# Kernel optimization log

Hardware: AMD Instinct MI355X
Metric: run time of the kernel (lower is better)

The kernel has to match this reference:

```python
import jax, jax.numpy as jnp
import numpy as np

N_EMBED = 768
NUM_HEADS = 12
HEAD_DIM = N_EMBED // NUM_HEADS
B, L = 4, 2048


def setup_inputs() -> dict:
    key = jax.random.key(0)
    ks = jax.random.split(key, 11)
    s = 0.02
    return {
        "key": jax.random.normal(ks[0], (B, L, N_EMBED), jnp.float32),
        "query": jax.random.normal(ks[1], (B, L, N_EMBED), jnp.float32),
        "value": jax.random.normal(ks[2], (B, L, N_EMBED), jnp.float32),
        "Wk": jax.random.normal(ks[3], (N_EMBED, N_EMBED), jnp.float32) * s,
        "bk": jnp.zeros((N_EMBED,), jnp.float32),
        "Wq": jax.random.normal(ks[4], (N_EMBED, N_EMBED), jnp.float32) * s,
        "bq": jnp.zeros((N_EMBED,), jnp.float32),
        "Wv": jax.random.normal(ks[5], (N_EMBED, N_EMBED), jnp.float32) * s,
        "bv": jnp.zeros((N_EMBED,), jnp.float32),
        "Wfc": jax.random.normal(ks[6], (N_EMBED, N_EMBED), jnp.float32) * s,
        "bfc": jnp.zeros((N_EMBED,), jnp.float32),
    }


def reference(key, query, value, Wk, bk, Wq, bq, Wv, bv, Wfc, bfc):
    # Linear projections (torch Linear: x @ W.T + b)
    k = key @ Wk.T + bk      # [B, Lk, D]
    q = query @ Wq.T + bq    # [B, Lq, D]
    v = value @ Wv.T + bv    # [B, Lv, D]
    Bsz, Lq = q.shape[0], q.shape[1]
    k = k.reshape(Bsz, -1, NUM_HEADS, HEAD_DIM)
    q = q.reshape(Bsz, Lq, NUM_HEADS, HEAD_DIM)
    v = v.reshape(Bsz, -1, NUM_HEADS, HEAD_DIM)
    # Full [B, H, Lq, Lk] score tensor, scaled by sqrt(n_embed) (faithful to source)
    energies = jnp.einsum("nqhd,nkhd->nhqk", q, k)
    attn = jax.nn.softmax(energies / jnp.sqrt(jnp.float32(N_EMBED)), axis=3)
    out = jnp.einsum("nhql,nlhd->nqhd", attn, v).reshape(Bsz, Lq, N_EMBED)
    return out @ Wfc.T + bfc
```

## Files before the change

### kernel.cpp

```cpp
#include <hip/hip_runtime.h>
#include <hip/hip_bf16.h>

#define NEMB 768
#define NH   12
#define HD   64
#define BSZ  4
#define SEQ  2048
#define MTOT (BSZ * SEQ)

typedef short bf16x8 __attribute__((ext_vector_type(8)));
typedef short short4v __attribute__((ext_vector_type(4)));
typedef float f32x4 __attribute__((ext_vector_type(4)));

__device__ __forceinline__ short f2bf(float f) {
  unsigned u = __builtin_bit_cast(unsigned, f);
  u += 0x7FFFu + ((u >> 16) & 1u);
  return (short)(u >> 16);
}

__device__ __forceinline__ void g2l16(const short* g, short* l) {
  __builtin_amdgcn_global_load_lds((const __attribute__((address_space(1))) unsigned*)g,
                                   (__attribute__((address_space(3))) unsigned*)l, 16, 0, 0);
}

__device__ __forceinline__ int swz(int x) { return (x ^ (x >> 3)) & 7; }

__global__ __launch_bounds__(256) void cvt3(const float* __restrict__ a0, const float* __restrict__ a1,
                                            const float* __restrict__ a2, short* __restrict__ o0,
                                            short* __restrict__ o1, short* __restrict__ o2) {
  const float* in; short* out;
  switch (blockIdx.y) { case 0: in = a0; out = o0; break;
                        case 1: in = a1; out = o1; break;
                        default: in = a2; out = o2; }
  int i = blockIdx.x * 256 + threadIdx.x;
  float4 f = reinterpret_cast<const float4*>(in)[i];
  short4v s; s[0] = f2bf(f.x); s[1] = f2bf(f.y); s[2] = f2bf(f.z); s[3] = f2bf(f.w);
  reinterpret_cast<short4v*>(out)[i] = s;
}

__global__ __launch_bounds__(256) void cvt4(const float* __restrict__ a0, const float* __restrict__ a1,
                                            const float* __restrict__ a2, const float* __restrict__ a3,
                                            short* __restrict__ o0, short* __restrict__ o1,
                                            short* __restrict__ o2, short* __restrict__ o3) {
  const float* in; short* out;
  switch (blockIdx.y) { case 0: in = a0; out = o0; break;
                        case 1: in = a1; out = o1; break;
                        case 2: in = a2; out = o2; break;
                        default: in = a3; out = o3; }
  int i = blockIdx.x * 256 + threadIdx.x;
  float4 f = reinterpret_cast<const float4*>(in)[i];
  short4v s; s[0] = f2bf(f.x); s[1] = f2bf(f.y); s[2] = f2bf(f.z); s[3] = f2bf(f.w);
  reinterpret_cast<short4v*>(out)[i] = s;
}

template <int OUTBF>
__global__ __launch_bounds__(256) void gemm_nt(const short* __restrict__ A, const short* __restrict__ W,
                                               const float* __restrict__ bias, void* __restrict__ Cout) {
  __shared__ __align__(16) short As[128 * 32];
  __shared__ __align__(16) short Bs[128 * 32];
  const int tid = threadIdx.x;
  const int lane = tid & 63, w = tid >> 6;
  const int wr = w >> 1, wc = w & 1;
  const int l15 = lane & 15, l4 = lane >> 4;
  const int m0 = blockIdx.x * 128, n0 = blockIdx.y * 128;

  f32x4 acc[4][4] = {};

  for (int k0 = 0; k0 < NEMB; k0 += 32) {
    __syncthreads();
#pragma unroll
    for (int i = 0; i < 2; ++i) {
      const int idx = tid + i * 256;
      const int row = idx >> 2, u = idx & 3;
      g2l16(A + (size_t)(m0 + row) * NEMB + k0 + u * 8, &As[idx * 8]);
      g2l16(W + (size_t)(n0 + row) * NEMB + k0 + u * 8, &Bs[idx * 8]);
    }
    __syncthreads();

    bf16x8 af[4], bfr[4];
#pragma unroll
    for (int m = 0; m < 4; ++m)
      af[m] = *reinterpret_cast<const bf16x8*>(&As[(wr * 64 + m * 16 + l15) * 32 + l4 * 8]);
#pragma unroll
    for (int n = 0; n < 4; ++n)
      bfr[n] = *reinterpret_cast<const bf16x8*>(&Bs[(wc * 64 + n * 16 + l15) * 32 + l4 * 8]);
#pragma unroll
    for (int m = 0; m < 4; ++m)
#pragma unroll
      for (int n = 0; n < 4; ++n)
        acc[m][n] = __builtin_amdgcn_mfma_f32_16x16x32_bf16(af[m], bfr[n], acc[m][n], 0, 0, 0);
  }

  float bj[4];
#pragma unroll
  for (int n = 0; n < 4; ++n) bj[n] = bias[n0 + wc * 64 + n * 16 + l15];
#pragma unroll
  for (int m = 0; m < 4; ++m)
#pragma unroll
    for (int n = 0; n < 4; ++n) {
      const int col = n0 + wc * 64 + n * 16 + l15;
#pragma unroll
      for (int r = 0; r < 4; ++r) {
        const int row = m0 + wr * 64 + m * 16 + l4 * 4 + r;
        const float v = acc[m][n][r] + bj[n];
        if (OUTBF) reinterpret_cast<short*>(Cout)[(size_t)row * NEMB + col] = f2bf(v);
        else       reinterpret_cast<float*>(Cout)[(size_t)row * NEMB + col] = v;
      }
    }
}

__global__ __launch_bounds__(256) void attn_mfma(const short* __restrict__ qp, const short* __restrict__ kp,
                                                 const short* __restrict__ vp, short* __restrict__ ao) {
  __shared__ __align__(16) short Ks[64 * 64];
  __shared__ __align__(16) short Vt[64 * 64];
  __shared__ __align__(16) short Ps[4][16 * 72];
  const int tid = threadIdx.x, lane = tid & 63, w = tid >> 6;
  const int l15 = lane & 15, l4 = lane >> 4;
  const int q0 = blockIdx.x * 64;
  const int bh = blockIdx.y, b = bh / NH, h = bh % NH;
  const size_t abase = (size_t)b * SEQ * NEMB + h * HD;

  bf16x8 qf[2];
#pragma unroll
  for (int kb = 0; kb < 2; ++kb)
    qf[kb] = *reinterpret_cast<const bf16x8*>(
        &qp[abase + (size_t)(q0 + w * 16 + l15) * NEMB + kb * 32 + l4 * 8]);

  f32x4 o[4] = {};
  float lacc[4] = {0.f, 0.f, 0.f, 0.f};
  const float scale = 0.036084391824351615f;
  const int vd8 = tid & 7, vkv2 = tid >> 3;

  for (int kt = 0; kt < SEQ / 64; ++kt) {
    __syncthreads();
#pragma unroll
    for (int i = 0; i < 2; ++i) {
      const int idx = tid + i * 256;
      const int row = idx >> 3, u = idx & 7;
      g2l16(kp + abase + (size_t)(kt * 64 + row) * NEMB + (u ^ swz(row)) * 8, &Ks[idx * 8]);
    }
    {
      const short* vr = vp + abase + (size_t)(kt * 64 + vkv2 * 2) * NEMB + vd8 * 8;
      bf16x8 v0 = *reinterpret_cast<const bf16x8*>(vr);
      bf16x8 v1 = *reinterpret_cast<const bf16x8*>(vr + NEMB);
      const int u = vkv2 >> 2, sub = vkv2 & 3;
#pragma unroll
      for (int j = 0; j < 8; ++j) {
        const int d = vd8 * 8 + j;
        unsigned pack = (unsigned)(unsigned short)v0[j] | ((unsigned)(unsigned short)v1[j] << 16);
        *reinterpret_cast<unsigned*>(reinterpret_cast<char*>(Vt) + d * 128 + (u ^ swz(d)) * 16 + sub * 4) = pack;
      }
    }
    __syncthreads();

    f32x4 sf[4];
#pragma unroll
    for (int nf = 0; nf < 4; ++nf) {
      f32x4 a = {0.f, 0.f, 0.f, 0.f};
#pragma unroll
      for (int kb = 0; kb < 2; ++kb) {
        const int row = nf * 16 + l15;
        const int u = kb * 4 + l4;
        bf16x8 kf = *reinterpret_cast<const bf16x8*>(
            reinterpret_cast<char*>(Ks) + row * 128 + (u ^ swz(row)) * 16);
        a = __builtin_amdgcn_mfma_f32_16x16x32_bf16(qf[kb], kf, a, 0, 0, 0);
      }
      sf[nf] = a;
    }

#pragma unroll
    for (int nf = 0; nf < 4; ++nf)
#pragma unroll
      for (int r = 0; r < 4; ++r) {
        const float p = __expf(sf[nf][r] * scale);
        lacc[r] += p;
        Ps[w][(l4 * 4 + r) * 72 + nf * 16 + l15] = f2bf(p);
      }

#pragma unroll
    for (int kb = 0; kb < 2; ++kb) {
      bf16x8 pf = *reinterpret_cast<const bf16x8*>(&Ps[w][l15 * 72 + kb * 32 + l4 * 8]);
#pragma unroll
      for (int df = 0; df < 4; ++df) {
        const int d = df * 16 + l15;
        const int u = kb * 4 + l4;
        bf16x8 vf = *reinterpret_cast<const bf16x8*>(
            reinterpret_cast<char*>(Vt) + d * 128 + (u ^ swz(d)) * 16);
        o[df] = __builtin_amdgcn_mfma_f32_16x16x32_bf16(pf, vf, o[df], 0, 0, 0);
      }
    }
  }

#pragma unroll
  for (int r = 0; r < 4; ++r)
#pragma unroll
    for (int off = 1; off < 16; off <<= 1)
      lacc[r] += __shfl_xor(lacc[r], off, 64);

#pragma unroll
  for (int df = 0; df < 4; ++df)
#pragma unroll
    for (int r = 0; r < 4; ++r) {
      const int row = q0 + w * 16 + l4 * 4 + r;
      ao[abase + (size_t)row * NEMB + df * 16 + l15] = f2bf(o[df][r] / lacc[r]);
    }
}

extern "C" void kernel_launch(void* const* d_in, const int* in_sizes, int n_in,
                              void* d_out, int out_size, void* d_ws, size_t ws_size,
                              hipStream_t stream) {
  const float* key   = (const float*)d_in[0];
  const float* query = (const float*)d_in[1];
  const float* value = (const float*)d_in[2];
  const float* Wk    = (const float*)d_in[3];
  const float* bk    = (const float*)d_in[4];
  const float* Wq    = (const float*)d_in[5];
  const float* bq    = (const float*)d_in[6];
  const float* Wv    = (const float*)d_in[7];
  const float* bv    = (const float*)d_in[8];
  const float* Wfc   = (const float*)d_in[9];
  const float* bfc   = (const float*)d_in[10];

  const size_t P = (size_t)MTOT * NEMB;
  const size_t WSZ = (size_t)NEMB * NEMB;
  short* ws  = (short*)d_ws;
  short* qb  = ws;
  short* kb2 = qb + P;
  short* vb2 = kb2 + P;
  short* wq  = vb2 + P;
  short* wk  = wq + WSZ;
  short* wv  = wk + WSZ;
  short* wf  = wv + WSZ;
  short* qpp = wf + WSZ;
  short* kpp = qpp + P;
  short* vpp = kpp + P;
  short* aop = vpp + P;

  cvt3<<<dim3(P / 4 / 256, 3), 256, 0, stream>>>(query, key, value, qb, kb2, vb2);
  cvt4<<<dim3(WSZ / 4 / 256, 4), 256, 0, stream>>>(Wq, Wk, Wv, Wfc, wq, wk, wv, wf);

  dim3 gg(MTOT / 128, NEMB / 128);
  gemm_nt<1><<<gg, 256, 0, stream>>>(qb,  wq, bq, qpp);
  gemm_nt<1><<<gg, 256, 0, stream>>>(kb2, wk, bk, kpp);
  gemm_nt<1><<<gg, 256, 0, stream>>>(vb2, wv, bv, vpp);
  attn_mfma<<<dim3(SEQ / 64, BSZ * NH), 256, 0, stream>>>(qpp, kpp, vpp, aop);
  gemm_nt<0><<<gg, 256, 0, stream>>>(aop, wf, bfc, d_out);
}
```

Baseline: 322.4 us.

## Merge launches, fold softmax scale into Q projection, and swizzle attention LDS

Collapses the two conversion kernels into one launch and the three QKV projection GEMMs into a single z-indexed launch. The softmax scale times log2(e) is folded into the Q projection epilogue so attention can use exp2f directly. Attention also gets an XCD-aware block remap, V loads issued before the barrier, perm-based V transpose packing, an XOR-swizzled P buffer to cut LDS bank conflicts, and a reciprocal instead of a per-element divide. Rounding Q after scaling slightly changes numerics, and the merged conversion grid launches many idle blocks for the weight matrices.

```diff
diff --git a/kernel.cpp b/kernel.cpp
--- a/kernel.cpp
+++ b/kernel.cpp
@@ -1,5 +1,6 @@
 #include <hip/hip_runtime.h>
 #include <hip/hip_bf16.h>
+#include <math.h>
 
 #define NEMB 768
 #define NH   12
@@ -8,14 +9,16 @@
 #define SEQ  2048
 #define MTOT (BSZ * SEQ)
 
+#define SCALE_LOG2E 0.0520587833f
+
 typedef short bf16x8 __attribute__((ext_vector_type(8)));
 typedef short short4v __attribute__((ext_vector_type(4)));
 typedef float f32x4 __attribute__((ext_vector_type(4)));
+typedef unsigned u32x4 __attribute__((ext_vector_type(4)));
 
 __device__ __forceinline__ short f2bf(float f) {
-  unsigned u = __builtin_bit_cast(unsigned, f);
-  u += 0x7FFFu + ((u >> 16) & 1u);
-  return (short)(u >> 16);
+  __bf16 h = (__bf16)f;
+  return __builtin_bit_cast(short, h);
 }
 
 __device__ __forceinline__ void g2l16(const short* g, short* l) {
@@ -25,37 +28,97 @@
 
 __device__ __forceinline__ int swz(int x) { return (x ^ (x >> 3)) & 7; }
 
-__global__ __launch_bounds__(256) void cvt3(const float* __restrict__ a0, const float* __restrict__ a1,
-                                            const float* __restrict__ a2, short* __restrict__ o0,
-                                            short* __restrict__ o1, short* __restrict__ o2) {
-  const float* in; short* out;
-  switch (blockIdx.y) { case 0: in = a0; out = o0; break;
-                        case 1: in = a1; out = o1; break;
-                        default: in = a2; out = o2; }
+__global__ __launch_bounds__(256) void cvt_all(
+    const float* __restrict__ i0, const float* __restrict__ i1, const float* __restrict__ i2,
+    const float* __restrict__ i3, const float* __restrict__ i4, const float* __restrict__ i5,
+    const float* __restrict__ i6,
+    short* __restrict__ o0, short* __restrict__ o1, short* __restrict__ o2,
+    short* __restrict__ o3, short* __restrict__ o4, short* __restrict__ o5,
+    short* __restrict__ o6) {
+  const int ACT4 = (MTOT * NEMB) / 4;
+  const int WGT4 = (NEMB * NEMB) / 4;
+  const float* in; short* out; int n4;
+  switch (blockIdx.y) {
+    case 0: in = i0; out = o0; n4 = ACT4; break;
+    case 1: in = i1; out = o1; n4 = ACT4; break;
+    case 2: in = i2; out = o2; n4 = ACT4; break;
+    case 3: in = i3; out = o3; n4 = WGT4; break;
+    case 4: in = i4; out = o4; n4 = WGT4; break;
+    case 5: in = i5; out = o5; n4 = WGT4; break;
+    default: in = i6; out = o6; n4 = WGT4; break;
+  }
   int i = blockIdx.x * 256 + threadIdx.x;
+  if (i >= n4) return;
   float4 f = reinterpret_cast<const float4*>(in)[i];
   short4v s; s[0] = f2bf(f.x); s[1] = f2bf(f.y); s[2] = f2bf(f.z); s[3] = f2bf(f.w);
   reinterpret_cast<short4v*>(out)[i] = s;
 }
 
-__global__ __launch_bounds__(256) void cvt4(const float* __restrict__ a0, const float* __restrict__ a1,
-                                            const float* __restrict__ a2, const float* __restrict__ a3,
-                                            short* __restrict__ o0, short* __restrict__ o1,
-                                            short* __restrict__ o2, short* __restrict__ o3) {
-  const float* in; short* out;
-  switch (blockIdx.y) { case 0: in = a0; out = o0; break;
-                        case 1: in = a1; out = o1; break;
-                        case 2: in = a2; out = o2; break;
-                        default: in = a3; out = o3; }
-  int i = blockIdx.x * 256 + threadIdx.x;
-  float4 f = reinterpret_cast<const float4*>(in)[i];
-  short4v s; s[0] = f2bf(f.x); s[1] = f2bf(f.y); s[2] = f2bf(f.z); s[3] = f2bf(f.w);
-  reinterpret_cast<short4v*>(out)[i] = s;
-}
-
-template <int OUTBF>
-__global__ __launch_bounds__(256) void gemm_nt(const short* __restrict__ A, const short* __restrict__ W,
-                                               const float* __restrict__ bias, void* __restrict__ Cout) {
+__global__ __launch_bounds__(256) void gemm_qkv(
+    const short* __restrict__ A0, const short* __restrict__ A1, const short* __restrict__ A2,
+    const short* __restrict__ W0, const short* __restrict__ W1, const short* __restrict__ W2,
+    const float* __restrict__ b0, const float* __restrict__ b1, const float* __restrict__ b2,
+    short* __restrict__ O0, short* __restrict__ O1, short* __restrict__ O2) {
+  __shared__ __align__(16) short As[128 * 32];
+  __shared__ __align__(16) short Bs[128 * 32];
+  const short* A; const short* W; const float* bias; short* O; float scl;
+  switch (blockIdx.z) {
+    case 0:  A = A0; W = W0; bias = b0; O = O0; scl = SCALE_LOG2E; break;
+    case 1:  A = A1; W = W1; bias = b1; O = O1; scl = 1.f; break;
+    default: A = A2; W = W2; bias = b2; O = O2; scl = 1.f; break;
+  }
+  const int tid = threadIdx.x;
+  const int lane = tid & 63, w = tid >> 6;
+  const int wr = w >> 1, wc = w & 1;
+  const int l15 = lane & 15, l4 = lane >> 4;
+  const int m0 = blockIdx.x * 128, n0 = blockIdx.y * 128;
+
+  f32x4 acc[4][4] = {};
+
+  for (int k0 = 0; k0 < NEMB; k0 += 32) {
+    __syncthreads();
+#pragma unroll
+    for (int i = 0; i < 2; ++i) {
+      const int idx = tid + i * 256;
+      const int row = idx >> 2, u = idx & 3;
+      g2l16(A + (size_t)(m0 + row) * NEMB + k0 + u * 8, &As[idx * 8]);
+      g2l16(W + (size_t)(n0 + row) * NEMB + k0 + u * 8, &Bs[idx * 8]);
+    }
+    __syncthreads();
+
+    bf16x8 af[4], bfr[4];
+#pragma unroll
+    for (int m = 0; m < 4; ++m)
+      af[m] = *reinterpret_cast<const bf16x8*>(&As[(wr * 64 + m * 16 + l15) * 32 + l4 * 8]);
+#pragma unroll
+    for (int n = 0; n < 4; ++n)
+      bfr[n] = *reinterpret_cast<const bf16x8*>(&Bs[(wc * 64 + n * 16 + l15) * 32 + l4 * 8]);
+#pragma unroll
+    for (int m = 0; m < 4; ++m)
+#pragma unroll
+      for (int n = 0; n < 4; ++n)
+        acc[m][n] = __builtin_amdgcn_mfma_f32_16x16x32_bf16(af[m], bfr[n], acc[m][n], 0, 0, 0);
+  }
+
+  float bj[4];
+#pragma unroll
+  for (int n = 0; n < 4; ++n) bj[n] = bias[n0 + wc * 64 + n * 16 + l15];
+#pragma unroll
+  for (int m = 0; m < 4; ++m)
+#pragma unroll
+    for (int n = 0; n < 4; ++n) {
+      const int col = n0 + wc * 64 + n * 16 + l15;
+#pragma unroll
+      for (int r = 0; r < 4; ++r) {
+        const int row = m0 + wr * 64 + m * 16 + l4 * 4 + r;
+        O[(size_t)row * NEMB + col] = f2bf((acc[m][n][r] + bj[n]) * scl);
+      }
+    }
+}
+
+__global__ __launch_bounds__(256) void gemm_fc(
+    const short* __restrict__ A, const short* __restrict__ W,
+    const float* __restrict__ bias, float* __restrict__ C) {
   __shared__ __align__(16) short As[128 * 32];
   __shared__ __align__(16) short Bs[128 * 32];
   const int tid = threadIdx.x;
@@ -102,9 +165,7 @@
 #pragma unroll
       for (int r = 0; r < 4; ++r) {
         const int row = m0 + wr * 64 + m * 16 + l4 * 4 + r;
-        const float v = acc[m][n][r] + bj[n];
-        if (OUTBF) reinterpret_cast<short*>(Cout)[(size_t)row * NEMB + col] = f2bf(v);
-        else       reinterpret_cast<float*>(Cout)[(size_t)row * NEMB + col] = v;
+        C[(size_t)row * NEMB + col] = acc[m][n][r] + bj[n];
       }
     }
 }
@@ -116,8 +177,11 @@
   __shared__ __align__(16) short Ps[4][16 * 72];
   const int tid = threadIdx.x, lane = tid & 63, w = tid >> 6;
   const int l15 = lane & 15, l4 = lane >> 4;
-  const int q0 = blockIdx.x * 64;
-  const int bh = blockIdx.y, b = bh / NH, h = bh % NH;
+  const int wg = blockIdx.x;
+  const int nid = (wg & 7) * 192 + (wg >> 3);
+  const int q0 = (nid & 31) * 64;
+  const int bh = nid >> 5;
+  const int b = bh / NH, h = bh - b * NH;
   const size_t abase = (size_t)b * SEQ * NEMB + h * HD;
 
   bf16x8 qf[2];
@@ -128,11 +192,16 @@
 
   f32x4 o[4] = {};
   float lacc[4] = {0.f, 0.f, 0.f, 0.f};
-  const float scale = 0.036084391824351615f;
   const int vd8 = tid & 7, vkv2 = tid >> 3;
+  const int vu = vkv2 >> 2, vsub = vkv2 & 3;
+  const int pch = l15 >> 3, pcl = l15 & 7;
 
   for (int kt = 0; kt < SEQ / 64; ++kt) {
-    __syncthreads();
+    const short* vr = vp + abase + (size_t)(kt * 64 + vkv2 * 2) * NEMB + vd8 * 8;
+    bf16x8 v0 = *reinterpret_cast<const bf16x8*>(vr);
+    bf16x8 v1 = *reinterpret_cast<const bf16x8*>(vr + NEMB);
+    __syncthreads();
+
 #pragma unroll
     for (int i = 0; i < 2; ++i) {
       const int idx = tid + i * 256;
@@ -140,15 +209,15 @@
       g2l16(kp + abase + (size_t)(kt * 64 + row) * NEMB + (u ^ swz(row)) * 8, &Ks[idx * 8]);
     }
     {
-      const short* vr = vp + abase + (size_t)(kt * 64 + vkv2 * 2) * NEMB + vd8 * 8;
-      bf16x8 v0 = *reinterpret_cast<const bf16x8*>(vr);
-      bf16x8 v1 = *reinterpret_cast<const bf16x8*>(vr + NEMB);
-      const int u = vkv2 >> 2, sub = vkv2 & 3;
-#pragma unroll
-      for (int j = 0; j < 8; ++j) {
-        const int d = vd8 * 8 + j;
-        unsigned pack = (unsigned)(unsigned short)v0[j] | ((unsigned)(unsigned short)v1[j] << 16);
-        *reinterpret_cast<unsigned*>(reinterpret_cast<char*>(Vt) + d * 128 + (u ^ swz(d)) * 16 + sub * 4) = pack;
+      u32x4 a0 = __builtin_bit_cast(u32x4, v0);
+      u32x4 a1 = __builtin_bit_cast(u32x4, v1);
+#pragma unroll
+      for (int jj = 0; jj < 4; ++jj) {
+        unsigned lo = __builtin_amdgcn_perm(a1[jj], a0[jj], 0x05040100u);
+        unsigned hi = __builtin_amdgcn_perm(a1[jj], a0[jj], 0x07060302u);
+        const int d0 = vd8 * 8 + jj * 2;
+        *reinterpret_cast<unsigned*>(reinterpret_cast<char*>(Vt) + d0 * 128 + (vu ^ swz(d0)) * 16 + vsub * 4) = lo;
+        *reinterpret_cast<unsigned*>(reinterpret_cast<char*>(Vt) + (d0 + 1) * 128 + (vu ^ swz(d0 + 1)) * 16 + vsub * 4) = hi;
       }
     }
     __syncthreads();
@@ -172,14 +241,15 @@
     for (int nf = 0; nf < 4; ++nf)
 #pragma unroll
       for (int r = 0; r < 4; ++r) {
-        const float p = __expf(sf[nf][r] * scale);
+        const float p = exp2f(sf[nf][r]);
         lacc[r] += p;
-        Ps[w][(l4 * 4 + r) * 72 + nf * 16 + l15] = f2bf(p);
+        Ps[w][(l4 * 4 + r) * 72 + (((nf * 2 + pch) ^ l4) << 3) + pcl] = f2bf(p);
       }
 
 #pragma unroll
     for (int kb = 0; kb < 2; ++kb) {
-      bf16x8 pf = *reinterpret_cast<const bf16x8*>(&Ps[w][l15 * 72 + kb * 32 + l4 * 8]);
+      bf16x8 pf = *reinterpret_cast<const bf16x8*>(
+          &Ps[w][l15 * 72 + (((kb * 4 + l4) ^ ((l15 >> 2) & 3)) << 3)]);
 #pragma unroll
       for (int df = 0; df < 4; ++df) {
         const int d = df * 16 + l15;
@@ -197,12 +267,16 @@
     for (int off = 1; off < 16; off <<= 1)
       lacc[r] += __shfl_xor(lacc[r], off, 64);
 
+  float inv[4];
+#pragma unroll
+  for (int r = 0; r < 4; ++r) inv[r] = 1.f / lacc[r];
+
 #pragma unroll
   for (int df = 0; df < 4; ++df)
 #pragma unroll
     for (int r = 0; r < 4; ++r) {
       const int row = q0 + w * 16 + l4 * 4 + r;
-      ao[abase + (size_t)row * NEMB + df * 16 + l15] = f2bf(o[df][r] / lacc[r]);
+      ao[abase + (size_t)row * NEMB + df * 16 + l15] = f2bf(o[df][r] * inv[r]);
     }
 }
 
@@ -236,13 +310,13 @@
   short* vpp = kpp + P;
   short* aop = vpp + P;
 
-  cvt3<<<dim3(P / 4 / 256, 3), 256, 0, stream>>>(query, key, value, qb, kb2, vb2);
-  cvt4<<<dim3(WSZ / 4 / 256, 4), 256, 0, stream>>>(Wq, Wk, Wv, Wfc, wq, wk, wv, wf);
-
-  dim3 gg(MTOT / 128, NEMB / 128);
-  gemm_nt<1><<<gg, 256, 0, stream>>>(qb,  wq, bq, qpp);
-  gemm_nt<1><<<gg, 256, 0, stream>>>(kb2, wk, bk, kpp);
-  gemm_nt<1><<<gg, 256, 0, stream>>>(vb2, wv, bv, vpp);
-  attn_mfma<<<dim3(SEQ / 64, BSZ * NH), 256, 0, stream>>>(qpp, kpp, vpp, aop);
-  gemm_nt<0><<<gg, 256, 0, stream>>>(aop, wf, bfc, d_out);
-}
+  cvt_all<<<dim3(P / 4 / 256, 7), 256, 0, stream>>>(
+      query, key, value, Wq, Wk, Wv, Wfc, qb, kb2, vb2, wq, wk, wv, wf);
+
+  gemm_qkv<<<dim3(MTOT / 128, NEMB / 128, 3), 256, 0, stream>>>(
+      qb, kb2, vb2, wq, wk, wv, bq, bk, bv, qpp, kpp, vpp);
+
+  attn_mfma<<<dim3((SEQ / 64) * BSZ * NH), 256, 0, stream>>>(qpp, kpp, vpp, aop);
+
+  gemm_fc<<<dim3(MTOT / 128, NEMB / 128), 256, 0, stream>>>(aop, wf, bfc, (float*)d_out);
+}
```

After: 308.4 us. 4.3% less time.
